# Kernel optimization log

Hardware: AMD Instinct MI355X
Metric: run time of the kernel (lower is better)

Reference implementation:

```python
import jax, jax.numpy as jnp
import numpy as np

D_MODEL = 1024
NUM_HEADS = 16
D_K = D_MODEL // NUM_HEADS  # 64
THETA = 10000.0


def setup_inputs() -> dict:
    key = jax.random.key(0)
    k_x, k_q, k_k, k_v, k_o = jax.random.split(key, 5)
    B, S = 2, 2048
    std = (2.0 / (D_MODEL + D_MODEL)) ** 0.5
    x = jax.random.normal(k_x, (B, S, D_MODEL), dtype=jnp.float32)
    Wq = std * jax.random.truncated_normal(k_q, -3.0, 3.0, (D_MODEL, D_MODEL), dtype=jnp.float32)
    Wk = std * jax.random.truncated_normal(k_k, -3.0, 3.0, (D_MODEL, D_MODEL), dtype=jnp.float32)
    Wv = std * jax.random.truncated_normal(k_v, -3.0, 3.0, (D_MODEL, D_MODEL), dtype=jnp.float32)
    Wo = std * jax.random.truncated_normal(k_o, -3.0, 3.0, (D_MODEL, D_MODEL), dtype=jnp.float32)
    return {"x": x, "Wq": Wq, "Wk": Wk, "Wv": Wv, "Wo": Wo}


def _apply_rope(t, cos, sin):
    # t: [B, H, S, d_k]; cos/sin: [S, d_k//2] broadcast over B, H
    tr = t.reshape(*t.shape[:-1], D_K // 2, 2)
    t1, t2 = tr[..., 0], tr[..., 1]
    r1 = t1 * cos - t2 * sin
    r2 = t1 * sin + t2 * cos
    return jnp.stack([r1, r2], axis=-1).reshape(t.shape)


def reference(x, Wq, Wk, Wv, Wo):
    B, S, D = x.shape
    H, dk = NUM_HEADS, D_K
    # projections (no bias): y = x @ W.T
    Q = (x @ Wq.T).reshape(B, S, H, dk).transpose(0, 2, 1, 3)  # [B,H,S,dk]
    K = (x @ Wk.T).reshape(B, S, H, dk).transpose(0, 2, 1, 3)
    V = (x @ Wv.T).reshape(B, S, H, dk).transpose(0, 2, 1, 3)
    # RoPE angles for positions 0..S-1
    pos = jnp.arange(S, dtype=jnp.float32)[:, None]            # [S,1]
    freqs = 1.0 / (THETA ** (jnp.arange(0, dk, 2, dtype=jnp.float32) / dk))  # [dk/2]
    angles = pos * freqs[None, :]                              # [S, dk/2]
    cos, sin = jnp.cos(angles), jnp.sin(angles)
    Q = _apply_rope(Q, cos, sin)
    K = _apply_rope(K, cos, sin)
    # causal scaled dot-product attention
    scores = jnp.einsum("bhqd,bhkd->bhqk", Q, K) / jnp.sqrt(jnp.float32(dk))
    causal = jnp.tril(jnp.ones((S, S), dtype=bool))
    scores = jnp.where(causal, scores, -jnp.inf)
    probs = jax.nn.softmax(scores, axis=-1)
    attn = jnp.einsum("bhqk,bhkd->bhqd", probs, V)             # [B,H,S,dk]
    attn = attn.transpose(0, 2, 1, 3).reshape(B, S, H * dk)
    return attn @ Wo.T
```

## Files before the change

### kernel.cpp

```cpp
#include <hip/hip_runtime.h>
#include <hip/hip_bf16.h>

typedef __bf16 bf16;
typedef __bf16 bf16x8 __attribute__((ext_vector_type(8)));
typedef float f32x4 __attribute__((ext_vector_type(4)));

#define MFMA16(A, B, C) __builtin_amdgcn_mfma_f32_16x16x32_bf16((A), (B), (C), 0, 0, 0)

static __device__ __forceinline__ void gload16(const bf16* g, bf16* l) {
    __builtin_amdgcn_global_load_lds((const __attribute__((address_space(1))) void*)g,
                                     (__attribute__((address_space(3))) void*)l, 16, 0, 0);
}

__global__ void detect_kernel(const void* w, int* flag) {
    float v = (float)((const bf16*)w)[threadIdx.x];
    unsigned long long bad = __ballot(!(fabsf(v) < 1.0f));
    if (threadIdx.x == 0) *flag = bad ? 1 : 0;
}

__global__ __launch_bounds__(256) void convert_all(const void* x, const void* w0,
                                                   const void* w1, const void* w2,
                                                   const void* w3, bf16* xb, bf16* b0,
                                                   bf16* b1, bf16* b2, bf16* b3,
                                                   const int* flagp) {
    if (*flagp == 0) return;
    int id = (blockIdx.x * 256 + threadIdx.x) * 4;
    const int XN = 1 << 22;
    const float* src;
    bf16* dst;
    int off;
    if (id < XN) {
        src = (const float*)x; dst = xb; off = id;
    } else {
        int r = id - XN;
        int wi = r >> 20;
        off = r & ((1 << 20) - 1);
        src = (const float*)(wi == 0 ? w0 : wi == 1 ? w1 : wi == 2 ? w2 : w3);
        dst = (wi == 0 ? b0 : wi == 1 ? b1 : wi == 2 ? b2 : b3);
    }
    float4 v = *(const float4*)(src + off);
    bf16 o[4] = {(bf16)v.x, (bf16)v.y, (bf16)v.z, (bf16)v.w};
    *(uint2*)(dst + off) = *(uint2*)o;
}

template <int MODE>
__global__ __launch_bounds__(128, 3) void gemm_nt(const void* rawA, const bf16* convA,
                                                  const void* rW0, const bf16* cW0,
                                                  const void* rW1, const bf16* cW1,
                                                  const void* rW2, const bf16* cW2,
                                                  bf16* Qo, bf16* Ko, bf16* Vt,
                                                  void* Cout, const int* flagp) {
    const int K = 1024;
    __shared__ __attribute__((aligned(16))) bf16 lsA[2][128 * 32];
    __shared__ __attribute__((aligned(16))) bf16 lsB[2][64 * 32];
    const int flag = *flagp;
    const bf16* A = flag ? convA : (const bf16*)rawA;
    int tensor, n0;
    const bf16* W;
    if (MODE == 0) {
        tensor = blockIdx.x >> 4;
        n0 = (blockIdx.x & 15) * 64;
        W = tensor == 0 ? (flag ? cW0 : (const bf16*)rW0)
          : tensor == 1 ? (flag ? cW1 : (const bf16*)rW1)
                        : (flag ? cW2 : (const bf16*)rW2);
    } else {
        tensor = 0;
        n0 = blockIdx.x * 64;
        W = flag ? cW0 : (const bf16*)rW0;
    }
    const int t = threadIdx.x;
    const int m0 = blockIdx.y * 128;
    const int w = t >> 6, lane = t & 63;
    const int llo = lane & 15, quad = lane >> 4;
    const int sel = (llo >> 1) & 3;

    f32x4 acc[4][4] = {};

    auto stage = [&](int k0, int buf) {
#pragma unroll
        for (int j = 0; j < 4; ++j) {
            int c = j * 128 + t;
            int row = c >> 2, pos = c & 3;
            int g = pos ^ ((row >> 1) & 3);
            gload16(A + (size_t)(m0 + row) * K + k0 + g * 8, &lsA[buf][c * 8]);
        }
#pragma unroll
        for (int j = 0; j < 2; ++j) {
            int c = j * 128 + t;
            int row = c >> 2, pos = c & 3;
            int g = pos ^ ((row >> 1) & 3);
            gload16(W + (size_t)(n0 + row) * K + k0 + g * 8, &lsB[buf][c * 8]);
        }
    };

    auto compute = [&](int buf) {
        bf16x8 a[4], bb[4];
#pragma unroll
        for (int mi = 0; mi < 4; ++mi) {
            int r = w * 64 + mi * 16 + llo;
            a[mi] = *(const bf16x8*)&lsA[buf][r * 32 + ((quad ^ sel) * 8)];
        }
#pragma unroll
        for (int ni = 0; ni < 4; ++ni) {
            int r = ni * 16 + llo;
            bb[ni] = *(const bf16x8*)&lsB[buf][r * 32 + ((quad ^ sel) * 8)];
        }
#pragma unroll
        for (int mi = 0; mi < 4; ++mi)
#pragma unroll
            for (int ni = 0; ni < 4; ++ni)
                acc[mi][ni] = MFMA16(a[mi], bb[ni], acc[mi][ni]);
    };

    stage(0, 0);
    for (int it = 0; it < 32; it += 2) {
        __syncthreads();
        stage((it + 1) * 32, 1);
        compute(0);
        __syncthreads();
        if (it + 2 < 32) stage((it + 2) * 32, 0);
        compute(1);
    }

#pragma unroll
    for (int mi = 0; mi < 4; ++mi)
#pragma unroll
        for (int ni = 0; ni < 4; ++ni)
#pragma unroll
            for (int r = 0; r < 4; ++r) {
                int row = m0 + w * 64 + mi * 16 + quad * 4 + r;
                int col = n0 + ni * 16 + llo;
                float v = acc[mi][ni][r];
                if (MODE == 1) {
                    if (flag)
                        ((float*)Cout)[(size_t)row * 1024 + col] = v;
                    else
                        ((bf16*)Cout)[(size_t)row * 1024 + col] = (bf16)v;
                } else if (tensor == 2) {
                    int b = row >> 11, s = row & 2047;
                    Vt[((size_t)b * 1024 + col) * 2048 + s] = (bf16)v;
                } else {
                    int d = col & 63, s = row & 2047;
                    float partner = __shfl_xor(v, 1);
                    float freq = exp2f((float)(d >> 1) * -0.4152410118609203f);
                    float rev = (float)s * freq * 0.15915494309189535f;
                    rev -= floorf(rev);
                    float sn = __builtin_amdgcn_sinf(rev);
                    float cs = __builtin_amdgcn_cosf(rev);
                    float outv = v * cs + partner * sn * ((d & 1) ? 1.0f : -1.0f);
                    bf16* dst = (tensor == 0) ? Qo : Ko;
                    dst[(size_t)row * 1024 + col] = (bf16)outv;
                }
            }
}

__global__ __launch_bounds__(256, 2) void attn_kernel(const bf16* __restrict__ Q,
                                                      const bf16* __restrict__ Kr,
                                                      const bf16* __restrict__ Vt,
                                                      bf16* __restrict__ O) {
    __shared__ __attribute__((aligned(16))) bf16 lsK[2][64 * 64];
    __shared__ __attribute__((aligned(16))) bf16 lsV[2][64 * 64];
    __shared__ __attribute__((aligned(16))) bf16 lsP[4][32 * 64];
    const int blk = blockIdx.x;
    const int u = blk >> 5;
    const int ib = (u < 8) ? (15 - u) : (u - 8);
    const int bh = blk & 31;
    const int b = bh >> 4, h = bh & 15;
    const int t = threadIdx.x, w = t >> 6, lane = t & 63;
    const int llo = lane & 15, quad = lane >> 4;
    const int q0w = ib * 128 + w * 32;

    bf16x8 aQ[2][2];
#pragma unroll
    for (int qi = 0; qi < 2; ++qi) {
        const size_t qb =
            ((size_t)(b * 2048 + q0w + qi * 16 + llo)) * 1024 + h * 64 + quad * 8;
        aQ[qi][0] = *(const bf16x8*)&Q[qb];
        aQ[qi][1] = *(const bf16x8*)&Q[qb + 32];
    }

    f32x4 o[2][4] = {};
    float lpart[2] = {0.f, 0.f};
    const float SC = 0.18033688011112042f;
    const int qlane0 = q0w + llo;

    const int srow8 = lane >> 3;
    const int sc = (lane & 7) ^ srow8;
    const int nch = 2 * ib + 2;

    auto stage = [&](int tt, int buf) {
        const int kv0 = tt * 64;
#pragma unroll
        for (int jj = 0; jj < 2; ++jj) {
            int seg = w + jj * 4;
            int rowk = seg * 8 + srow8;
            gload16(&Kr[((size_t)(b * 2048 + kv0 + rowk)) * 1024 + h * 64 + sc * 8],
                    &lsK[buf][seg * 512 + lane * 8]);
            gload16(&Vt[((size_t)(b * 1024 + h * 64 + rowk)) * 2048 + kv0 + sc * 8],
                    &lsV[buf][seg * 512 + lane * 8]);
        }
    };

    stage(0, 0);

    for (int tt = 0; tt < nch; ++tt) {
        const int cur = tt & 1;
        const int kv0 = tt * 64;
        __syncthreads();
        if (tt + 1 < nch) stage(tt + 1, cur ^ 1);

        if (kv0 <= q0w + 31) {
            bf16x8 kf[4][2];
#pragma unroll
            for (int half = 0; half < 4; ++half) {
                int rk = half * 16 + llo;
                kf[half][0] = *(const bf16x8*)&lsK[cur][rk * 64 + ((quad ^ (rk & 7)) * 8)];
                kf[half][1] =
                    *(const bf16x8*)&lsK[cur][rk * 64 + (((quad + 4) ^ (rk & 7)) * 8)];
            }
            bf16x8 vf[2][4];
#pragma unroll
            for (int kc = 0; kc < 2; ++kc)
#pragma unroll
                for (int g = 0; g < 4; ++g) {
                    int rv = g * 16 + llo;
                    int cg = kc * 4 + quad;
                    vf[kc][g] =
                        *(const bf16x8*)&lsV[cur][rv * 64 + ((cg ^ (rv & 7)) * 8)];
                }

            const bool need_mask = (kv0 + 63 >= q0w);
#pragma unroll
            for (int qi = 0; qi < 2; ++qi) {
                const int q = qlane0 + qi * 16;
                const int prow = qi * 16 + llo;
#pragma unroll
                for (int half = 0; half < 4; ++half) {
                    f32x4 z = {};
                    z = MFMA16(kf[half][0], aQ[qi][0], z);
                    z = MFMA16(kf[half][1], aQ[qi][1], z);
                    union { bf16 hh[4]; uint2 uu; } pk;
                    if (need_mask) {
                        int kvb = kv0 + half * 16 + quad * 4;
#pragma unroll
                        for (int r = 0; r < 4; ++r) {
                            float e = (kvb + r <= q) ? z[r] * SC : -INFINITY;
                            float p = exp2f(e);
                            lpart[qi] += p;
                            pk.hh[r] = (bf16)p;
                        }
                    } else {
#pragma unroll
                        for (int r = 0; r < 4; ++r) {
                            float p = exp2f(z[r] * SC);
                            lpart[qi] += p;
                            pk.hh[r] = (bf16)p;
                        }
                    }
                    int cw = 2 * half + (quad >> 1);
                    *(uint2*)&lsP[w][prow * 64 + ((cw ^ (llo & 7)) * 8) + (quad & 1) * 4] =
                        pk.uu;
                }
            }
            __builtin_amdgcn_wave_barrier();
#pragma unroll
            for (int qi = 0; qi < 2; ++qi) {
                const int prow = qi * 16 + llo;
#pragma unroll
                for (int kc = 0; kc < 2; ++kc) {
                    int cr = 4 * kc + quad;
                    bf16x8 aP =
                        *(const bf16x8*)&lsP[w][prow * 64 + ((cr ^ (llo & 7)) * 8)];
#pragma unroll
                    for (int g = 0; g < 4; ++g) o[qi][g] = MFMA16(aP, vf[kc][g], o[qi][g]);
                }
            }
            __builtin_amdgcn_wave_barrier();
        }
    }

    float lfull[2];
#pragma unroll
    for (int qi = 0; qi < 2; ++qi) {
        float l = lpart[qi];
        l += __shfl_xor(l, 16);
        l += __shfl_xor(l, 32);
        lfull[qi] = l;
    }
#pragma unroll
    for (int qi = 0; qi < 2; ++qi)
#pragma unroll
        for (int r = 0; r < 4; ++r) {
            float l = __shfl(lfull[qi], (lane & 48) | (quad * 4 + r));
            float inv = 1.f / l;
            int q = q0w + qi * 16 + quad * 4 + r;
            size_t ob = ((size_t)(b * 2048 + q)) * 1024 + h * 64;
#pragma unroll
            for (int g = 0; g < 4; ++g)
                O[ob + g * 16 + llo] = (bf16)(o[qi][g][r] * inv);
        }
}

extern "C" void kernel_launch(void* const* d_in, const int* in_sizes, int n_in,
                              void* d_out, int out_size, void* d_ws, size_t ws_size,
                              hipStream_t stream) {
    const size_t TN = (size_t)4096 * 1024;

    int* flag = (int*)d_ws;
    bf16* Q = (bf16*)((char*)d_ws + 256);
    bf16* Kb = Q + TN;
    bf16* Vt = Kb + TN;
    bf16* xb = Vt + TN;
    bf16* Wb0 = xb + TN;
    bf16* Wb1 = Wb0 + TN / 4;
    bf16* Wb2 = Wb1 + TN / 4;
    bf16* Wb3 = Wb2 + TN / 4;
    bf16* AO = Q;

    detect_kernel<<<1, 64, 0, stream>>>(d_in[1], flag);
    convert_all<<<8192, 256, 0, stream>>>(d_in[0], d_in[1], d_in[2], d_in[3], d_in[4],
                                          xb, Wb0, Wb1, Wb2, Wb3, flag);

    gemm_nt<0><<<dim3(48, 32), 128, 0, stream>>>(d_in[0], xb, d_in[1], Wb0, d_in[2],
                                                 Wb1, d_in[3], Wb2, Q, Kb, Vt, nullptr,
                                                 flag);

    attn_kernel<<<512, 256, 0, stream>>>(Q, Kb, Vt, AO);

    gemm_nt<1><<<dim3(16, 32), 128, 0, stream>>>(AO, AO, d_in[4], Wb3, nullptr,
                                                 nullptr, nullptr, nullptr, nullptr,
                                                 nullptr, nullptr, d_out, flag);
}
```

Measured before the change: 224.3 us.

## Split KV range for long causal query blocks and merge with a combine kernel

Query blocks in the upper half of the sequence (ib>=8) now have their KV range split across two workgroups. Each half writes unnormalized partial outputs and row sums into reused workspace, and a new combine kernel adds the halves and normalizes them. The goal is to even out per-block work in the causal attention and shorten the tail of the longest blocks. The change also raises launch_bounds occupancy to 3 and swaps exp2f for the hardware exp2 builtin, at the cost of an extra kernel launch, extra global traffic, and partial outputs rounded to bf16.

Result: faster. 204.7 us (-8.8%).

```diff
diff --git a/kernel.cpp b/kernel.cpp
--- a/kernel.cpp
+++ b/kernel.cpp
@@ -154,17 +154,35 @@
             }
 }
 
-__global__ __launch_bounds__(256, 2) void attn_kernel(const bf16* __restrict__ Q,
+__global__ __launch_bounds__(256, 3) void attn_kernel(const bf16* __restrict__ Q,
                                                       const bf16* __restrict__ Kr,
                                                       const bf16* __restrict__ Vt,
-                                                      bf16* __restrict__ O) {
+                                                      bf16* __restrict__ O,
+                                                      bf16* __restrict__ Opart,
+                                                      float* __restrict__ lws) {
     __shared__ __attribute__((aligned(16))) bf16 lsK[2][64 * 64];
     __shared__ __attribute__((aligned(16))) bf16 lsV[2][64 * 64];
     __shared__ __attribute__((aligned(16))) bf16 lsP[4][32 * 64];
     const int blk = blockIdx.x;
-    const int u = blk >> 5;
-    const int ib = (u < 8) ? (15 - u) : (u - 8);
-    const int bh = blk & 31;
+    int ib, bh, s, tt0, tt1;
+    bool split;
+    if (blk < 512) {
+        split = true;
+        s = blk >> 8;
+        int c = blk & 255;
+        ib = 15 - (c >> 5);
+        bh = c & 31;
+        tt0 = s ? (ib + 1) : 0;
+        tt1 = s ? (2 * ib + 1) : ib;
+    } else {
+        split = false;
+        s = 0;
+        int c = blk - 512;
+        ib = c >> 5;
+        bh = c & 31;
+        tt0 = 0;
+        tt1 = 2 * ib + 1;
+    }
     const int b = bh >> 4, h = bh & 15;
     const int t = threadIdx.x, w = t >> 6, lane = t & 63;
     const int llo = lane & 15, quad = lane >> 4;
@@ -186,7 +204,6 @@
 
     const int srow8 = lane >> 3;
     const int sc = (lane & 7) ^ srow8;
-    const int nch = 2 * ib + 2;
 
     auto stage = [&](int tt, int buf) {
         const int kv0 = tt * 64;
@@ -201,13 +218,13 @@
         }
     };
 
-    stage(0, 0);
-
-    for (int tt = 0; tt < nch; ++tt) {
-        const int cur = tt & 1;
+    stage(tt0, 0);
+
+    for (int tt = tt0; tt <= tt1; ++tt) {
+        const int cur = (tt - tt0) & 1;
         const int kv0 = tt * 64;
         __syncthreads();
-        if (tt + 1 < nch) stage(tt + 1, cur ^ 1);
+        if (tt + 1 <= tt1) stage(tt + 1, cur ^ 1);
 
         if (kv0 <= q0w + 31) {
             bf16x8 kf[4][2];
@@ -245,14 +262,14 @@
 #pragma unroll
                         for (int r = 0; r < 4; ++r) {
                             float e = (kvb + r <= q) ? z[r] * SC : -INFINITY;
-                            float p = exp2f(e);
+                            float p = __builtin_amdgcn_exp2f(e);
                             lpart[qi] += p;
                             pk.hh[r] = (bf16)p;
                         }
                     } else {
 #pragma unroll
                         for (int r = 0; r < 4; ++r) {
-                            float p = exp2f(z[r] * SC);
+                            float p = __builtin_amdgcn_exp2f(z[r] * SC);
                             lpart[qi] += p;
                             pk.hh[r] = (bf16)p;
                         }
@@ -287,18 +304,54 @@
         l += __shfl_xor(l, 32);
         lfull[qi] = l;
     }
-#pragma unroll
-    for (int qi = 0; qi < 2; ++qi)
-#pragma unroll
-        for (int r = 0; r < 4; ++r) {
-            float l = __shfl(lfull[qi], (lane & 48) | (quad * 4 + r));
-            float inv = 1.f / l;
-            int q = q0w + qi * 16 + quad * 4 + r;
-            size_t ob = ((size_t)(b * 2048 + q)) * 1024 + h * 64;
-#pragma unroll
-            for (int g = 0; g < 4; ++g)
-                O[ob + g * 16 + llo] = (bf16)(o[qi][g][r] * inv);
-        }
+
+    if (split) {
+        const int slot = ((ib - 8) * 32 + bh) * 2 + s;
+        bf16* op = Opart + (size_t)slot * 8192;
+#pragma unroll
+        for (int qi = 0; qi < 2; ++qi) {
+#pragma unroll
+            for (int r = 0; r < 4; ++r) {
+                int row_in = w * 32 + qi * 16 + quad * 4 + r;
+#pragma unroll
+                for (int g = 0; g < 4; ++g)
+                    op[row_in * 64 + g * 16 + llo] = (bf16)o[qi][g][r];
+            }
+            if (quad == 0) lws[slot * 128 + w * 32 + qi * 16 + llo] = lfull[qi];
+        }
+    } else {
+#pragma unroll
+        for (int qi = 0; qi < 2; ++qi)
+#pragma unroll
+            for (int r = 0; r < 4; ++r) {
+                float l = __shfl(lfull[qi], (lane & 48) | (quad * 4 + r));
+                float inv = 1.f / l;
+                int q = q0w + qi * 16 + quad * 4 + r;
+                size_t ob = ((size_t)(b * 2048 + q)) * 1024 + h * 64;
+#pragma unroll
+                for (int g = 0; g < 4; ++g)
+                    O[ob + g * 16 + llo] = (bf16)(o[qi][g][r] * inv);
+            }
+    }
+}
+
+__global__ __launch_bounds__(256) void combine_kernel(const bf16* __restrict__ Opart,
+                                                      const float* __restrict__ lws,
+                                                      bf16* __restrict__ AO) {
+    int id = blockIdx.x * 256 + threadIdx.x;
+    int d = id & 63;
+    int h = (id >> 6) & 15;
+    int qoff = (id >> 10) & 1023;
+    int b = id >> 20;
+    int ib8 = qoff >> 7;
+    int q_in = qoff & 127;
+    int slot = (ib8 * 32 + (b * 16 + h)) * 2;
+    size_t base = (size_t)slot * 8192 + q_in * 64 + d;
+    float o0 = (float)Opart[base];
+    float o1 = (float)Opart[base + 8192];
+    float l = lws[slot * 128 + q_in] + lws[(slot + 1) * 128 + q_in];
+    int q = 1024 + qoff;
+    AO[((size_t)(b * 2048 + q)) * 1024 + h * 64 + d] = (bf16)((o0 + o1) / l);
 }
 
 extern "C" void kernel_launch(void* const* d_in, const int* in_sizes, int n_in,
@@ -316,6 +369,8 @@
     bf16* Wb2 = Wb1 + TN / 4;
     bf16* Wb3 = Wb2 + TN / 4;
     bf16* AO = Q;
+    bf16* Opart = xb;
+    float* lws = (float*)Wb0;
 
     detect_kernel<<<1, 64, 0, stream>>>(d_in[1], flag);
     convert_all<<<8192, 256, 0, stream>>>(d_in[0], d_in[1], d_in[2], d_in[3], d_in[4],
@@ -325,7 +380,8 @@
                                                  Wb1, d_in[3], Wb2, Q, Kb, Vt, nullptr,
                                                  flag);
 
-    attn_kernel<<<512, 256, 0, stream>>>(Q, Kb, Vt, AO);
+    attn_kernel<<<768, 256, 0, stream>>>(Q, Kb, Vt, AO, Opart, lws);
+    combine_kernel<<<8192, 256, 0, stream>>>(Opart, lws, AO);
 
     gemm_nt<1><<<dim3(16, 32), 128, 0, stream>>>(AO, AO, d_in[4], Wb3, nullptr,
                                                  nullptr, nullptr, nullptr, nullptr,
```
